# Performance work log

Hardware: AMD Instinct MI355X
Metric: run time of the kernel (lower is better)

Reference implementation:

```python
import jax, jax.numpy as jnp
import numpy as np

B, K = 64, 1000
TEMP = 4.0
LAMBDA_OT = 0.5
EPS = 0.05
MAX_ITER = 50
THRESH = 1e-3
CLAMP_MIN = 1e-8


def setup_inputs() -> dict:
    key = jax.random.key(0)
    k1, k2, k3 = jax.random.split(key, 3)
    student_logits = jax.random.normal(k1, (B, K), dtype=jnp.float32)
    teacher_logits = jax.random.normal(k2, (B, K), dtype=jnp.float32)
    labels = jax.random.randint(k3, (B,), 0, K)
    # cost_type='uniform': C_ij = 1 - delta_ij
    C = (jnp.ones((K, K)) - jnp.eye(K)).astype(jnp.float32)
    return {"student_logits": student_logits, "teacher_logits": teacher_logits,
            "labels": labels, "C": C}


def _log_sinkhorn(log_a, log_b, C):
    # log_a, log_b: (B, K); C: (K, K)
    M = C[None, :, :] / EPS                      # (1, K, K)
    la = log_a[:, :, None]                       # (B, K, 1)
    lb = log_b[:, None, :]                       # (B, 1, K)
    f0 = jnp.zeros_like(log_a)
    g0 = jnp.zeros_like(log_b)

    def step(carry, _):
        f, g, done = carry
        f_new = -jax.scipy.special.logsumexp(g[:, None, :] - M + lb, axis=2)
        g_new = -jax.scipy.special.logsumexp(f_new[:, :, None] - M + la, axis=1)
        err = jnp.max(jnp.abs(f_new - f))
        # emulate the torch early-break: once converged, freeze f, g
        f2 = jnp.where(done, f, f_new)
        g2 = jnp.where(done, g, g_new)
        done2 = jnp.logical_or(done, err < THRESH)
        return (f2, g2, done2), None

    (f, g, _), _ = jax.lax.scan(step, (f0, g0, jnp.array(False)), None, length=MAX_ITER)
    log_pi = f[:, :, None] + g[:, None, :] - M + la + lb   # (B, K, K)
    pi = jnp.exp(log_pi)
    cost = jnp.mean(jnp.sum(C[None, :, :] * pi, axis=(1, 2)))
    return cost, pi


def reference(student_logits, teacher_logits, labels, C):
    p_T = jnp.maximum(jax.nn.softmax(teacher_logits / TEMP, axis=1), CLAMP_MIN)
    p_S = jnp.maximum(jax.nn.softmax(student_logits / TEMP, axis=1), CLAMP_MIN)
    ot_loss, transport_plan = _log_sinkhorn(jnp.log(p_T), jnp.log(p_S), C)
    # cross-entropy with integer labels (mean reduction)
    logp = jax.nn.log_softmax(student_logits, axis=1)
    ce_loss = -jnp.mean(jnp.take_along_axis(logp, labels[:, None], axis=1))
    total_loss = ce_loss + LAMBDA_OT * ot_loss
    return total_loss, ot_loss, ce_loss, transport_plan
```

## Files before the change

kernel.cpp:

```cpp
#include <hip/hip_runtime.h>
#include <math.h>

#define B_    64
#define K_    1000
#define KPL   16
#define MAXIT 50

#define C0 2.0611536e-09f
#define C1 (1.0f - C0)

#define SN_OFF 1024
#define AL_OFF 3300000
#define BE_OFF 3364000
#define ER_OFF 3428000
#define CE_OFF 3431200
#define CO_OFF 3431264

__device__ __forceinline__ float wsum(float v){
#pragma unroll
  for (int m = 32; m >= 1; m >>= 1) v += __shfl_xor(v, m, 64);
  return v;
}
__device__ __forceinline__ float wmax(float v){
#pragma unroll
  for (int m = 32; m >= 1; m >>= 1) v = fmaxf(v, __shfl_xor(v, m, 64));
  return v;
}
__device__ __forceinline__ float wmin(float v){
#pragma unroll
  for (int m = 32; m >= 1; m >>= 1) v = fminf(v, __shfl_xor(v, m, 64));
  return v;
}

__global__ __launch_bounds__(64) void k1_sinkhorn(
    const float* __restrict__ student, const float* __restrict__ teacher,
    const int* __restrict__ labels, float* __restrict__ outf)
{
  const int b = blockIdx.x;
  const int lane = threadIdx.x;

  float tl[KPL], sl[KPL], alpha[KPL], beta[KPL];
#pragma unroll
  for (int k = 0; k < KPL; ++k) {
    int idx = lane + 64 * k;
    bool own = idx < K_;
    tl[k] = own ? teacher[b * K_ + idx] : 0.f;
    sl[k] = own ? student[b * K_ + idx] : 0.f;
  }

  float m = -1e30f;
#pragma unroll
  for (int k = 0; k < KPL; ++k) { int idx = lane + 64*k; if (idx < K_) m = fmaxf(m, tl[k] * 0.25f); }
  m = wmax(m);
  float s = 0.f;
#pragma unroll
  for (int k = 0; k < KPL; ++k) {
    int idx = lane + 64*k;
    alpha[k] = (idx < K_) ? expf(tl[k] * 0.25f - m) : 0.f;
    s += alpha[k];
  }
  s = wsum(s);
  float inv = 1.0f / s;
#pragma unroll
  for (int k = 0; k < KPL; ++k) { int idx = lane + 64*k; alpha[k] = (idx < K_) ? fmaxf(alpha[k] * inv, 1e-8f) : 0.f; }

  m = -1e30f;
#pragma unroll
  for (int k = 0; k < KPL; ++k) { int idx = lane + 64*k; if (idx < K_) m = fmaxf(m, sl[k] * 0.25f); }
  m = wmax(m);
  s = 0.f;
#pragma unroll
  for (int k = 0; k < KPL; ++k) {
    int idx = lane + 64*k;
    beta[k] = (idx < K_) ? expf(sl[k] * 0.25f - m) : 0.f;
    s += beta[k];
  }
  s = wsum(s);
  inv = 1.0f / s;
#pragma unroll
  for (int k = 0; k < KPL; ++k) { int idx = lane + 64*k; beta[k] = (idx < K_) ? fmaxf(beta[k] * inv, 1e-8f) : 0.f; }

  float ms = -1e30f;
#pragma unroll
  for (int k = 0; k < KPL; ++k) { int idx = lane + 64*k; if (idx < K_) ms = fmaxf(ms, sl[k]); }
  ms = wmax(ms);
  float ss = 0.f;
#pragma unroll
  for (int k = 0; k < KPL; ++k) { int idx = lane + 64*k; if (idx < K_) ss += expf(sl[k] - ms); }
  ss = wsum(ss);
  float lse = ms + logf(ss);
  int lab = labels[b];
  float lv = -1e30f;
#pragma unroll
  for (int k = 0; k < KPL; ++k) { int idx = lane + 64*k; if (idx < K_ && idx == lab) lv = sl[k]; }
  lv = wmax(lv);
  if (lane == 0) outf[CE_OFF + b] = lv - lse;

#pragma unroll
  for (int k = 0; k < KPL; ++k) {
    int idx = lane + 64*k;
    if (idx < K_) { outf[AL_OFF + b * K_ + idx] = alpha[k]; outf[BE_OFF + b * K_ + idx] = beta[k]; }
  }

  float u[KPL], v[KPL], dprev[KPL];
#pragma unroll
  for (int k = 0; k < KPL; ++k) { u[k] = 1.f; v[k] = 1.f; dprev[k] = 1.f; }

  for (int t = 0; t < MAXIT; ++t) {
    float wl = 0.f;
#pragma unroll
    for (int k = 0; k < KPL; ++k) wl += v[k] * beta[k];
    float W = wsum(wl);

    float rmax = -1e30f, rmin = 1e30f;
#pragma unroll
    for (int k = 0; k < KPL; ++k) {
      float vb = v[k] * beta[k];
      float den = fmaf(C1, vb, C0 * W);
      float un = __builtin_amdgcn_rcpf(den);
      float r = un * dprev[k];
      int idx = lane + 64*k;
      if (idx < K_) { rmax = fmaxf(rmax, r); rmin = fminf(rmin, r); }
      dprev[k] = den;
      u[k] = un;
    }

#pragma unroll
    for (int k = 0; k < KPL; ++k) {
      int idx = lane + 64*k;
      if (idx < K_) outf[SN_OFF + t * (B_ * K_) + b * K_ + idx] = u[k];
    }

    float zl = 0.f;
#pragma unroll
    for (int k = 0; k < KPL; ++k) zl += u[k] * alpha[k];
    float Z = wsum(zl);
#pragma unroll
    for (int k = 0; k < KPL; ++k) {
      float ua = u[k] * alpha[k];
      v[k] = __builtin_amdgcn_rcpf(fmaf(C1, ua, C0 * Z));
    }

    rmax = wmax(rmax);
    rmin = wmin(rmin);
    if (lane == 0) {
      float err = fmaxf(fabsf(logf(rmax)), fabsf(logf(rmin)));
      outf[ER_OFF + t * B_ + b] = err;
    }
  }
}

__global__ __launch_bounds__(64) void k2_finalize(
    float* __restrict__ outf, float* __restrict__ X, float* __restrict__ Y)
{
  const int b = blockIdx.x;
  const int lane = threadIdx.x;

  int Tst = MAXIT - 1;
  bool found = false;
  for (int t = 0; t < MAXIT; ++t) {
    float e = outf[ER_OFF + t * B_ + lane];
    float me = wmax(e);
    if (!found && me < 0.001f) { Tst = t; found = true; }
  }

  float x[KPL], y[KPL];
  float zl = 0.f;
#pragma unroll
  for (int k = 0; k < KPL; ++k) {
    int idx = lane + 64*k;
    x[k] = (idx < K_) ? outf[SN_OFF + Tst * (B_ * K_) + b * K_ + idx] * outf[AL_OFF + b * K_ + idx] : 0.f;
    zl += x[k];
  }
  float Z = wsum(zl);

  float vs = 0.f, ds = 0.f;
#pragma unroll
  for (int k = 0; k < KPL; ++k) {
    int idx = lane + 64*k;
    float vv = __builtin_amdgcn_rcpf(fmaf(C1, x[k], C0 * Z));
    float be = (idx < K_) ? outf[BE_OFF + b * K_ + idx] : 0.f;
    y[k] = vv * be;
    vs += y[k];
    ds += x[k] * y[k];
    if (idx < K_) { X[b * K_ + idx] = x[k]; Y[b * K_ + idx] = y[k]; }
  }
  vs = wsum(vs);
  ds = wsum(ds);
  if (lane == 0) outf[CO_OFF + b] = C0 * (Z * vs - ds);
}

__global__ __launch_bounds__(64) void k2b_scalars(float* __restrict__ outf)
{
  const int lane = threadIdx.x;
  float ce = wsum(outf[CE_OFF + lane]);
  float co = wsum(outf[CO_OFF + lane]);
  if (lane == 0) {
    float cel = -ce * (1.0f / 64.0f);
    float ot  =  co * (1.0f / 64.0f);
    outf[0] = cel + 0.5f * ot;
    outf[1] = ot;
    outf[2] = cel;
  }
}

__global__ __launch_bounds__(256) void k3_pi(
    const float* __restrict__ X, const float* __restrict__ Y, float* __restrict__ outf)
{
  const int bid = blockIdx.x;
  const int b = bid / K_;
  const int i = bid - b * K_;
  const float x = X[b * K_ + i];
  const float* Yb = Y + b * K_;
  const size_t base = 3ull + (size_t)bid * K_;
  for (int j = threadIdx.x; j < K_; j += 256) {
    float val = x * Yb[j];
    if (j != i) val *= C0;
    outf[base + j] = val;
  }
}

extern "C" void kernel_launch(void* const* d_in, const int* in_sizes, int n_in,
                              void* d_out, int out_size, void* d_ws, size_t ws_size,
                              hipStream_t stream) {
  const float* student = (const float*)d_in[0];
  const float* teacher = (const float*)d_in[1];
  const int*   labels  = (const int*)d_in[2];
  float* outf = (float*)d_out;
  float* X = (float*)d_ws;
  float* Y = X + B_ * K_;

  k1_sinkhorn<<<B_, 64, 0, stream>>>(student, teacher, labels, outf);
  k2_finalize<<<B_, 64, 0, stream>>>(outf, X, Y);
  k2b_scalars<<<1, 64, 0, stream>>>(outf);
  k3_pi<<<B_ * K_, 256, 0, stream>>>(X, Y, outf);
}
```

Before: 371.0 us.

## Use DPP wave reductions, move CE to finalize, vectorize pi row stores

Replaces shuffle-based wave reductions with DPP row operations plus readlane. Drops the alpha/beta global stores from the serial Sinkhorn kernel and recomputes them (and the CE term) in the finalize kernel, shortening the latency-bound per-batch loop. Scratch error/CE/cost values move to workspace when it is large enough, and the finalize kernel finds the stop iteration with a ballot instead of a serial loop of reductions. The pi kernel writes each row as aligned float4 stores matched to the output's 3-element offset, in exchange for hard-coded alignment logic specific to K=1000.

```diff
diff --git a/kernel.cpp b/kernel.cpp
--- a/kernel.cpp
+++ b/kernel.cpp
@@ -10,31 +10,46 @@
 #define C1 (1.0f - C0)
 
 #define SN_OFF 1024
-#define AL_OFF 3300000
-#define BE_OFF 3364000
-#define ER_OFF 3428000
-#define CE_OFF 3431200
-#define CO_OFF 3431264
-
-__device__ __forceinline__ float wsum(float v){
-#pragma unroll
-  for (int m = 32; m >= 1; m >>= 1) v += __shfl_xor(v, m, 64);
-  return v;
-}
-__device__ __forceinline__ float wmax(float v){
-#pragma unroll
-  for (int m = 32; m >= 1; m >>= 1) v = fmaxf(v, __shfl_xor(v, m, 64));
-  return v;
-}
-__device__ __forceinline__ float wmin(float v){
-#pragma unroll
-  for (int m = 32; m >= 1; m >>= 1) v = fminf(v, __shfl_xor(v, m, 64));
-  return v;
+#define ER_OFF_FB 3428000
+#define CE_OFF_FB 3431200
+#define CO_OFF_FB 3431264
+
+__device__ __forceinline__ float wr_sum(float x) {
+  int xi;
+#define SSTEP(ctrl, rmask) \
+  xi = __float_as_int(x); \
+  x += __int_as_float(__builtin_amdgcn_update_dpp(0, xi, ctrl, rmask, 0xf, true));
+  SSTEP(0x111, 0xf) SSTEP(0x112, 0xf) SSTEP(0x114, 0xf) SSTEP(0x118, 0xf)
+  SSTEP(0x142, 0xa) SSTEP(0x143, 0xc)
+#undef SSTEP
+  return __int_as_float(__builtin_amdgcn_readlane(__float_as_int(x), 63));
+}
+__device__ __forceinline__ float wr_max(float x) {
+  int xi; float t;
+#define MSTEP(ctrl, rmask) \
+  xi = __float_as_int(x); \
+  t = __int_as_float(__builtin_amdgcn_update_dpp(xi, xi, ctrl, rmask, 0xf, false)); \
+  x = fmaxf(x, t);
+  MSTEP(0x111, 0xf) MSTEP(0x112, 0xf) MSTEP(0x114, 0xf) MSTEP(0x118, 0xf)
+  MSTEP(0x142, 0xa) MSTEP(0x143, 0xc)
+#undef MSTEP
+  return __int_as_float(__builtin_amdgcn_readlane(__float_as_int(x), 63));
+}
+__device__ __forceinline__ float wr_min(float x) {
+  int xi; float t;
+#define NSTEP(ctrl, rmask) \
+  xi = __float_as_int(x); \
+  t = __int_as_float(__builtin_amdgcn_update_dpp(xi, xi, ctrl, rmask, 0xf, false)); \
+  x = fminf(x, t);
+  NSTEP(0x111, 0xf) NSTEP(0x112, 0xf) NSTEP(0x114, 0xf) NSTEP(0x118, 0xf)
+  NSTEP(0x142, 0xa) NSTEP(0x143, 0xc)
+#undef NSTEP
+  return __int_as_float(__builtin_amdgcn_readlane(__float_as_int(x), 63));
 }
 
 __global__ __launch_bounds__(64) void k1_sinkhorn(
     const float* __restrict__ student, const float* __restrict__ teacher,
-    const int* __restrict__ labels, float* __restrict__ outf)
+    float* __restrict__ SN, float* __restrict__ ER)
 {
   const int b = blockIdx.x;
   const int lane = threadIdx.x;
@@ -51,7 +66,7 @@
   float m = -1e30f;
 #pragma unroll
   for (int k = 0; k < KPL; ++k) { int idx = lane + 64*k; if (idx < K_) m = fmaxf(m, tl[k] * 0.25f); }
-  m = wmax(m);
+  m = wr_max(m);
   float s = 0.f;
 #pragma unroll
   for (int k = 0; k < KPL; ++k) {
@@ -59,7 +74,7 @@
     alpha[k] = (idx < K_) ? expf(tl[k] * 0.25f - m) : 0.f;
     s += alpha[k];
   }
-  s = wsum(s);
+  s = wr_sum(s);
   float inv = 1.0f / s;
 #pragma unroll
   for (int k = 0; k < KPL; ++k) { int idx = lane + 64*k; alpha[k] = (idx < K_) ? fmaxf(alpha[k] * inv, 1e-8f) : 0.f; }
@@ -67,7 +82,7 @@
   m = -1e30f;
 #pragma unroll
   for (int k = 0; k < KPL; ++k) { int idx = lane + 64*k; if (idx < K_) m = fmaxf(m, sl[k] * 0.25f); }
-  m = wmax(m);
+  m = wr_max(m);
   s = 0.f;
 #pragma unroll
   for (int k = 0; k < KPL; ++k) {
@@ -75,32 +90,10 @@
     beta[k] = (idx < K_) ? expf(sl[k] * 0.25f - m) : 0.f;
     s += beta[k];
   }
-  s = wsum(s);
+  s = wr_sum(s);
   inv = 1.0f / s;
 #pragma unroll
   for (int k = 0; k < KPL; ++k) { int idx = lane + 64*k; beta[k] = (idx < K_) ? fmaxf(beta[k] * inv, 1e-8f) : 0.f; }
-
-  float ms = -1e30f;
-#pragma unroll
-  for (int k = 0; k < KPL; ++k) { int idx = lane + 64*k; if (idx < K_) ms = fmaxf(ms, sl[k]); }
-  ms = wmax(ms);
-  float ss = 0.f;
-#pragma unroll
-  for (int k = 0; k < KPL; ++k) { int idx = lane + 64*k; if (idx < K_) ss += expf(sl[k] - ms); }
-  ss = wsum(ss);
-  float lse = ms + logf(ss);
-  int lab = labels[b];
-  float lv = -1e30f;
-#pragma unroll
-  for (int k = 0; k < KPL; ++k) { int idx = lane + 64*k; if (idx < K_ && idx == lab) lv = sl[k]; }
-  lv = wmax(lv);
-  if (lane == 0) outf[CE_OFF + b] = lv - lse;
-
-#pragma unroll
-  for (int k = 0; k < KPL; ++k) {
-    int idx = lane + 64*k;
-    if (idx < K_) { outf[AL_OFF + b * K_ + idx] = alpha[k]; outf[BE_OFF + b * K_ + idx] = beta[k]; }
-  }
 
   float u[KPL], v[KPL], dprev[KPL];
 #pragma unroll
@@ -110,7 +103,7 @@
     float wl = 0.f;
 #pragma unroll
     for (int k = 0; k < KPL; ++k) wl += v[k] * beta[k];
-    float W = wsum(wl);
+    float W = wr_sum(wl);
 
     float rmax = -1e30f, rmin = 1e30f;
 #pragma unroll
@@ -128,73 +121,134 @@
 #pragma unroll
     for (int k = 0; k < KPL; ++k) {
       int idx = lane + 64*k;
-      if (idx < K_) outf[SN_OFF + t * (B_ * K_) + b * K_ + idx] = u[k];
+      if (idx < K_) SN[t * (B_ * K_) + b * K_ + idx] = u[k];
     }
 
     float zl = 0.f;
 #pragma unroll
     for (int k = 0; k < KPL; ++k) zl += u[k] * alpha[k];
-    float Z = wsum(zl);
+    float Z = wr_sum(zl);
 #pragma unroll
     for (int k = 0; k < KPL; ++k) {
       float ua = u[k] * alpha[k];
       v[k] = __builtin_amdgcn_rcpf(fmaf(C1, ua, C0 * Z));
     }
 
-    rmax = wmax(rmax);
-    rmin = wmin(rmin);
+    rmax = wr_max(rmax);
+    rmin = wr_min(rmin);
     if (lane == 0) {
       float err = fmaxf(fabsf(logf(rmax)), fabsf(logf(rmin)));
-      outf[ER_OFF + t * B_ + b] = err;
+      ER[t * B_ + b] = err;
     }
   }
 }
 
 __global__ __launch_bounds__(64) void k2_finalize(
-    float* __restrict__ outf, float* __restrict__ X, float* __restrict__ Y)
+    const float* __restrict__ student, const float* __restrict__ teacher,
+    const int* __restrict__ labels, const float* __restrict__ SN,
+    const float* __restrict__ ER, float* __restrict__ X, float* __restrict__ Y,
+    float* __restrict__ CE, float* __restrict__ CO)
 {
   const int b = blockIdx.x;
   const int lane = threadIdx.x;
 
-  int Tst = MAXIT - 1;
-  bool found = false;
-  for (int t = 0; t < MAXIT; ++t) {
-    float e = outf[ER_OFF + t * B_ + lane];
-    float me = wmax(e);
-    if (!found && me < 0.001f) { Tst = t; found = true; }
-  }
+  float mymax = 0.f;
+  if (lane < MAXIT) {
+    const float* e = ER + lane * B_;
+#pragma unroll 8
+    for (int bb = 0; bb < B_; ++bb) mymax = fmaxf(mymax, e[bb]);
+  }
+  unsigned long long ball = __ballot(lane < MAXIT && mymax < 0.001f);
+  int Tst = ball ? (int)__builtin_ctzll(ball) : (MAXIT - 1);
+
+  float tl[KPL], sl[KPL], alpha[KPL], beta[KPL];
+#pragma unroll
+  for (int k = 0; k < KPL; ++k) {
+    int idx = lane + 64 * k;
+    bool own = idx < K_;
+    tl[k] = own ? teacher[b * K_ + idx] : 0.f;
+    sl[k] = own ? student[b * K_ + idx] : 0.f;
+  }
+  float m = -1e30f;
+#pragma unroll
+  for (int k = 0; k < KPL; ++k) { int idx = lane + 64*k; if (idx < K_) m = fmaxf(m, tl[k] * 0.25f); }
+  m = wr_max(m);
+  float s = 0.f;
+#pragma unroll
+  for (int k = 0; k < KPL; ++k) {
+    int idx = lane + 64*k;
+    alpha[k] = (idx < K_) ? expf(tl[k] * 0.25f - m) : 0.f;
+    s += alpha[k];
+  }
+  s = wr_sum(s);
+  float inv = 1.0f / s;
+#pragma unroll
+  for (int k = 0; k < KPL; ++k) { int idx = lane + 64*k; alpha[k] = (idx < K_) ? fmaxf(alpha[k] * inv, 1e-8f) : 0.f; }
+
+  m = -1e30f;
+#pragma unroll
+  for (int k = 0; k < KPL; ++k) { int idx = lane + 64*k; if (idx < K_) m = fmaxf(m, sl[k] * 0.25f); }
+  m = wr_max(m);
+  s = 0.f;
+#pragma unroll
+  for (int k = 0; k < KPL; ++k) {
+    int idx = lane + 64*k;
+    beta[k] = (idx < K_) ? expf(sl[k] * 0.25f - m) : 0.f;
+    s += beta[k];
+  }
+  s = wr_sum(s);
+  inv = 1.0f / s;
+#pragma unroll
+  for (int k = 0; k < KPL; ++k) { int idx = lane + 64*k; beta[k] = (idx < K_) ? fmaxf(beta[k] * inv, 1e-8f) : 0.f; }
+
+  float ms = -1e30f;
+#pragma unroll
+  for (int k = 0; k < KPL; ++k) { int idx = lane + 64*k; if (idx < K_) ms = fmaxf(ms, sl[k]); }
+  ms = wr_max(ms);
+  float ss = 0.f;
+#pragma unroll
+  for (int k = 0; k < KPL; ++k) { int idx = lane + 64*k; if (idx < K_) ss += expf(sl[k] - ms); }
+  ss = wr_sum(ss);
+  float lse = ms + logf(ss);
+  int lab = labels[b];
+  float lv = -1e30f;
+#pragma unroll
+  for (int k = 0; k < KPL; ++k) { int idx = lane + 64*k; if (idx < K_ && idx == lab) lv = sl[k]; }
+  lv = wr_max(lv);
+  if (lane == 0) CE[b] = lv - lse;
 
   float x[KPL], y[KPL];
   float zl = 0.f;
-#pragma unroll
-  for (int k = 0; k < KPL; ++k) {
-    int idx = lane + 64*k;
-    x[k] = (idx < K_) ? outf[SN_OFF + Tst * (B_ * K_) + b * K_ + idx] * outf[AL_OFF + b * K_ + idx] : 0.f;
+  const float* SNrow = SN + Tst * (B_ * K_) + b * K_;
+#pragma unroll
+  for (int k = 0; k < KPL; ++k) {
+    int idx = lane + 64*k;
+    x[k] = (idx < K_) ? SNrow[idx] * alpha[k] : 0.f;
     zl += x[k];
   }
-  float Z = wsum(zl);
+  float Z = wr_sum(zl);
 
   float vs = 0.f, ds = 0.f;
 #pragma unroll
   for (int k = 0; k < KPL; ++k) {
     int idx = lane + 64*k;
     float vv = __builtin_amdgcn_rcpf(fmaf(C1, x[k], C0 * Z));
-    float be = (idx < K_) ? outf[BE_OFF + b * K_ + idx] : 0.f;
-    y[k] = vv * be;
+    y[k] = vv * beta[k];
     vs += y[k];
     ds += x[k] * y[k];
     if (idx < K_) { X[b * K_ + idx] = x[k]; Y[b * K_ + idx] = y[k]; }
   }
-  vs = wsum(vs);
-  ds = wsum(ds);
-  if (lane == 0) outf[CO_OFF + b] = C0 * (Z * vs - ds);
-}
-
-__global__ __launch_bounds__(64) void k2b_scalars(float* __restrict__ outf)
+  vs = wr_sum(vs);
+  ds = wr_sum(ds);
+  if (lane == 0) CO[b] = C0 * (Z * vs - ds);
+}
+
+__global__ __launch_bounds__(64) void k2b_scalars(
+    const float* __restrict__ CE, const float* __restrict__ CO, float* __restrict__ outf)
 {
   const int lane = threadIdx.x;
-  float ce = wsum(outf[CE_OFF + lane]);
-  float co = wsum(outf[CO_OFF + lane]);
+  float ce = wr_sum(CE[lane]);
+  float co = wr_sum(CO[lane]);
   if (lane == 0) {
     float cel = -ce * (1.0f / 64.0f);
     float ot  =  co * (1.0f / 64.0f);
@@ -210,13 +264,23 @@
   const int bid = blockIdx.x;
   const int b = bid / K_;
   const int i = bid - b * K_;
-  const float x = X[b * K_ + i];
+  const float x = X[bid];
   const float* Yb = Y + b * K_;
-  const size_t base = 3ull + (size_t)bid * K_;
-  for (int j = threadIdx.x; j < K_; j += 256) {
-    float val = x * Yb[j];
-    if (j != i) val *= C0;
-    outf[base + j] = val;
+  float* row = outf + 3 + (size_t)bid * (size_t)K_;
+  const int t = threadIdx.x;
+  if (t < 249) {
+    int j = 1 + 4 * t;
+    float4 val;
+    val.x = x * Yb[j+0] * ((j+0 == i) ? 1.0f : C0);
+    val.y = x * Yb[j+1] * ((j+1 == i) ? 1.0f : C0);
+    val.z = x * Yb[j+2] * ((j+2 == i) ? 1.0f : C0);
+    val.w = x * Yb[j+3] * ((j+3 == i) ? 1.0f : C0);
+    *(float4*)(row + j) = val;
+  } else if (t == 249) {
+    row[0]   = x * Yb[0]   * ((0   == i) ? 1.0f : C0);
+    row[997] = x * Yb[997] * ((997 == i) ? 1.0f : C0);
+    row[998] = x * Yb[998] * ((998 == i) ? 1.0f : C0);
+    row[999] = x * Yb[999] * ((999 == i) ? 1.0f : C0);
   }
 }
 
@@ -227,11 +291,25 @@
   const float* teacher = (const float*)d_in[1];
   const int*   labels  = (const int*)d_in[2];
   float* outf = (float*)d_out;
-  float* X = (float*)d_ws;
-  float* Y = X + B_ * K_;
-
-  k1_sinkhorn<<<B_, 64, 0, stream>>>(student, teacher, labels, outf);
-  k2_finalize<<<B_, 64, 0, stream>>>(outf, X, Y);
-  k2b_scalars<<<1, 64, 0, stream>>>(outf);
+  float* ws   = (float*)d_ws;
+
+  float* X = ws;
+  float* Y = ws + B_ * K_;
+  float *ER, *CE, *CO;
+  size_t need_bytes = (size_t)(2 * B_ * K_ + MAXIT * B_ + 2 * B_) * sizeof(float);
+  if (ws_size >= need_bytes) {
+    ER = ws + 2 * B_ * K_;
+    CE = ER + MAXIT * B_;
+    CO = CE + B_;
+  } else {
+    ER = outf + ER_OFF_FB;
+    CE = outf + CE_OFF_FB;
+    CO = outf + CO_OFF_FB;
+  }
+  float* SN = outf + SN_OFF;
+
+  k1_sinkhorn<<<B_, 64, 0, stream>>>(student, teacher, SN, ER);
+  k2_finalize<<<B_, 64, 0, stream>>>(student, teacher, labels, SN, ER, X, Y, CE, CO);
+  k2b_scalars<<<1, 64, 0, stream>>>(CE, CO, outf);
   k3_pi<<<B_ * K_, 256, 0, stream>>>(X, Y, outf);
 }
```

Result: faster. 348.1 us (-6.2%).
